# Performance work log

Measured on AMD Instinct MI355X. Metric: run time of the kernel, lower is better.

## Reference

```python
import jax, jax.numpy as jnp
import numpy as np


def setup_inputs() -> dict:
    key = jax.random.key(0)
    k_in, k_idx, k_neg, k_w, k_b = jax.random.split(key, 5)
    N, C_in, C_out, K, L = 8, 128, 256, 7, 16384
    x = jax.random.normal(k_in, (N, C_in, L), dtype=jnp.float32)
    idx = jax.random.randint(k_idx, (K, L), 0, L, dtype=jnp.int64)
    drop = jax.random.uniform(k_neg, (K, L)) < 0.05
    idx = jnp.where(drop, -1, idx)
    stdv = 1.0 / np.sqrt(C_in * K)
    weight = jax.random.uniform(k_w, (C_out, C_in, K), dtype=jnp.float32, minval=-stdv, maxval=stdv)
    bias = jax.random.uniform(k_b, (C_out,), dtype=jnp.float32, minval=-stdv, maxval=stdv)
    return {"input": x, "indices": idx, "weight": weight, "bias": bias}


def reference(input, indices, weight, bias):
    # indices: (K, L); -1 means zero-padding (matches utils.prepare_mask)
    mask = (indices >= 0).astype(input.dtype)          # (K, L)
    safe_idx = jnp.where(indices >= 0, indices, 0)     # (K, L)
    # im2col gather: (N, C_in, K, L), masked where neighbor is absent
    col = input[..., safe_idx] * mask
    # weight (C_out, C_in, K) contracted against col -> (N, C_out, L), mirrors bmm
    out = jnp.einsum('nckl,ock->nol', col, weight)
    out = out + bias[None, :, None]
    return out
```

## Files before the change

### kernel.cpp

```cpp
#include <hip/hip_runtime.h>
#include <stdint.h>

#define NB 8
#define CI 128
#define CO 256
#define KS 7
#define LL 16384
#define CK (CI * KS)

typedef _Float16 half8 __attribute__((ext_vector_type(8)));
typedef _Float16 half2v __attribute__((ext_vector_type(2)));
typedef float floatx4 __attribute__((ext_vector_type(4)));
typedef uint32_t uintx4 __attribute__((ext_vector_type(4)));

__device__ __forceinline__ void load16_to_lds(const void* g, void* l) {
    __builtin_amdgcn_global_load_lds(
        (const __attribute__((address_space(1))) void*)g,
        (__attribute__((address_space(3))) void*)l, 16, 0, 0);
}

__global__ __launch_bounds__(256) void convert_x(const float* __restrict__ x,
                                                 _Float16* __restrict__ xT) {
    __shared__ uint32_t tile[64][65];
    const int n  = blockIdx.y;
    const int l0 = blockIdx.x * 64;
    const int t  = threadIdx.x;
    const float* xs = x + (size_t)n * CI * LL + l0;

    const int l4  = (t & 15) * 4;
    const int cpr = t >> 4;
    #pragma unroll
    for (int p = 0; p < 4; ++p) {
        const int cp = cpr + p * 16;
        const float4 a4 = *(const float4*)(xs + (size_t)(2 * cp) * LL + l4);
        const float4 b4 = *(const float4*)(xs + (size_t)(2 * cp + 1) * LL + l4);
        half2v h;
        h[0] = (_Float16)a4.x; h[1] = (_Float16)b4.x;
        tile[l4 + 0][cp] = __builtin_bit_cast(uint32_t, h);
        h[0] = (_Float16)a4.y; h[1] = (_Float16)b4.y;
        tile[l4 + 1][cp] = __builtin_bit_cast(uint32_t, h);
        h[0] = (_Float16)a4.z; h[1] = (_Float16)b4.z;
        tile[l4 + 2][cp] = __builtin_bit_cast(uint32_t, h);
        h[0] = (_Float16)a4.w; h[1] = (_Float16)b4.w;
        tile[l4 + 3][cp] = __builtin_bit_cast(uint32_t, h);
    }
    __syncthreads();

    const int lw  = t >> 4;
    const int cp0 = (t & 15) * 4;
    _Float16* xd = xT + (size_t)n * LL * CI + (size_t)l0 * CI;
    #pragma unroll
    for (int p = 0; p < 4; ++p) {
        const int l = lw + p * 16;
        uintx4 d;
        d[0] = tile[l][cp0 + 0];
        d[1] = tile[l][cp0 + 1];
        d[2] = tile[l][cp0 + 2];
        d[3] = tile[l][cp0 + 3];
        *(uintx4*)(xd + (size_t)l * CI + cp0 * 2) = d;
    }
}

__global__ __launch_bounds__(256) void convert_w(const float* __restrict__ w,
                                                 _Float16* __restrict__ wT) {
    const int t = blockIdx.x * 256 + threadIdx.x;
    if (t >= CO * CK + 128) return;
    if (t >= CO * CK) { wT[t] = (_Float16)0.f; return; }
    const int o = t / CK;
    const int r = t - o * CK;
    const int k = r >> 7;
    const int c = r & 127;
    wT[t] = (_Float16)w[(size_t)o * CK + c * KS + k];
}

__global__ __launch_bounds__(256) void iconv_mfma(
    const _Float16* __restrict__ xT,
    const int*      __restrict__ idx,
    const _Float16* __restrict__ wT,
    const float*    __restrict__ bias,
    const _Float16* __restrict__ zrow,
    float*          __restrict__ out)
{
    __shared__ _Float16 a_lds[128 * 64];
    __shared__ _Float16 b_lds[128 * 64];

    const int l0 = blockIdx.x * 128;
    const int o0 = blockIdx.y * 128;
    const int n  = blockIdx.z;
    const int t  = threadIdx.x;
    const int lane = t & 63;
    const int wv = t >> 6;
    const int wo = (wv >> 1) * 64;
    const int wl = (wv & 1) * 64;
    const int m16 = lane & 15;
    const int q8  = (lane >> 4) * 8;

    floatx4 acc[4][4];
    #pragma unroll
    for (int i = 0; i < 4; ++i)
        #pragma unroll
        for (int j = 0; j < 4; ++j) acc[i][j] = (floatx4)0.f;

    const int srow = t >> 3;
    const int part = t & 7;

    int iv[KS][4];
    #pragma unroll
    for (int k = 0; k < KS; ++k)
        #pragma unroll
        for (int i = 0; i < 4; ++i)
            iv[k][i] = idx[k * LL + l0 + i * 32 + srow];

    const _Float16* xbase = xT + (size_t)n * LL * CI;
    const _Float16* wbase = wT + (size_t)(o0 + srow) * CK + part * 8;
    const int dst = srow * 64 + part * 8;

    for (int k = 0; k < KS; ++k) {
        for (int c0 = 0; c0 < CI; c0 += 64) {
            __syncthreads();
            #pragma unroll
            for (int i = 0; i < 4; ++i) {
                const int ii = iv[k][i];
                const _Float16* bs = (ii >= 0)
                    ? (xbase + (size_t)ii * CI + c0 + part * 8)
                    : (zrow + c0 + part * 8);
                load16_to_lds(bs, b_lds + i * 2048 + dst);
                load16_to_lds(wbase + (size_t)i * 32 * CK + k * CI + c0,
                              a_lds + i * 2048 + dst);
            }
            __syncthreads();

            #pragma unroll
            for (int kk = 0; kk < 2; ++kk) {
                half8 af[4], bf[4];
                #pragma unroll
                for (int mf = 0; mf < 4; ++mf)
                    af[mf] = *(const half8*)(a_lds + (wo + mf * 16 + m16) * 64 + kk * 32 + q8);
                #pragma unroll
                for (int nf = 0; nf < 4; ++nf)
                    bf[nf] = *(const half8*)(b_lds + (wl + nf * 16 + m16) * 64 + kk * 32 + q8);
                #pragma unroll
                for (int mf = 0; mf < 4; ++mf)
                    #pragma unroll
                    for (int nf = 0; nf < 4; ++nf)
                        acc[mf][nf] = __builtin_amdgcn_mfma_f32_16x16x32_f16(
                            af[mf], bf[nf], acc[mf][nf], 0, 0, 0);
            }
        }
    }

    const int r4 = (lane >> 4) * 4;
    #pragma unroll
    for (int mf = 0; mf < 4; ++mf) {
        const int obase = o0 + wo + mf * 16 + r4;
        const floatx4 b4 = *(const floatx4*)(bias + obase);
        #pragma unroll
        for (int nf = 0; nf < 4; ++nf) {
            const int l = l0 + wl + nf * 16 + m16;
            float* op = out + ((size_t)n * CO + obase) * LL + l;
            #pragma unroll
            for (int r = 0; r < 4; ++r)
                op[(size_t)r * LL] = acc[mf][nf][r] + b4[r];
        }
    }
}

__global__ __launch_bounds__(256) void iconv_fallback(
    const float* __restrict__ x, const int* __restrict__ idx,
    const float* __restrict__ w, const float* __restrict__ bias,
    float* __restrict__ out)
{
    __shared__ float col[CI][64];
    const int n  = blockIdx.y;
    const int l0 = blockIdx.x * 64;
    const int t  = threadIdx.x;
    const int ot = t & 63, lt = t >> 6;
    const int j = t >> 2, part = t & 3;
    float acc[4][16];
    #pragma unroll
    for (int oo = 0; oo < 4; ++oo) {
        const float bv = bias[ot * 4 + oo];
        #pragma unroll
        for (int ll = 0; ll < 16; ++ll) acc[oo][ll] = bv;
    }
    for (int k = 0; k < KS; ++k) {
        __syncthreads();
        const int i = idx[k * LL + l0 + j];
        const float* xr = x + (size_t)n * CI * LL;
        for (int q = 0; q < 32; ++q) {
            const int c = part * 32 + q;
            col[c][j] = (i >= 0) ? xr[(size_t)c * LL + i] : 0.f;
        }
        __syncthreads();
        for (int c = 0; c < CI; ++c) {
            const float* bv = &col[c][lt * 16];
            float wv[4];
            #pragma unroll
            for (int oo = 0; oo < 4; ++oo)
                wv[oo] = w[(size_t)(ot * 4 + oo) * CK + c * KS + k];
            #pragma unroll
            for (int oo = 0; oo < 4; ++oo)
                #pragma unroll
                for (int ll = 0; ll < 16; ++ll)
                    acc[oo][ll] += wv[oo] * bv[ll];
        }
    }
    #pragma unroll
    for (int oo = 0; oo < 4; ++oo) {
        float* orow = out + ((size_t)n * CO + (ot * 4 + oo)) * LL + l0 + lt * 16;
        #pragma unroll
        for (int q = 0; q < 16; ++q) orow[q] = acc[oo][q];
    }
}

extern "C" void kernel_launch(void* const* d_in, const int* in_sizes, int n_in,
                              void* d_out, int out_size, void* d_ws, size_t ws_size,
                              hipStream_t stream) {
    const float* x    = (const float*)d_in[0];
    const int*   idx  = (const int*)d_in[1];
    const float* w    = (const float*)d_in[2];
    const float* bias = (const float*)d_in[3];
    float* out = (float*)d_out;

    const size_t xt_bytes = (size_t)NB * LL * CI * sizeof(_Float16);
    const size_t wt_elems = (size_t)CO * CK + 128;
    const size_t need = xt_bytes + wt_elems * sizeof(_Float16);

    if (ws_size >= need) {
        _Float16* xT = (_Float16*)d_ws;
        _Float16* wT = (_Float16*)((char*)d_ws + xt_bytes);
        const _Float16* zr = wT + (size_t)CO * CK;
        convert_x<<<dim3(LL / 64, NB), 256, 0, stream>>>(x, xT);
        convert_w<<<dim3(((int)wt_elems + 255) / 256), 256, 0, stream>>>(w, wT);
        iconv_mfma<<<dim3(LL / 128, CO / 128, NB), 256, 0, stream>>>(
            xT, idx, wT, bias, zr, out);
    } else {
        iconv_fallback<<<dim3(LL / 64, NB), 256, 0, stream>>>(x, idx, w, bias, out);
    }
}
```

Measured before the change: 261.2 us.

## Double-buffer LDS tiles with swizzled layout and MFMA priority boost

Splits the A and B LDS tiles into two buffers so the global-to-LDS loads for the next K-chunk are issued before the MFMAs on the current chunk, with one barrier per iteration. Source chunks are XOR-swizzled by row so the half8 fragment reads hit fewer LDS bank conflicts, and s_setprio is raised around the MFMA block. The aim is to hide the gather latency and cut LDS conflicts. The cost is twice the LDS use (64KB per block), which may lower occupancy, and a fully unrolled 14-step loop that increases code size.

```diff
diff --git a/kernel.cpp b/kernel.cpp
--- a/kernel.cpp
+++ b/kernel.cpp
@@ -81,8 +81,8 @@
     const _Float16* __restrict__ zrow,
     float*          __restrict__ out)
 {
-    __shared__ _Float16 a_lds[128 * 64];
-    __shared__ _Float16 b_lds[128 * 64];
+    __shared__ _Float16 a_lds[2][128 * 64];
+    __shared__ _Float16 b_lds[2][128 * 64];
 
     const int l0 = blockIdx.x * 128;
     const int o0 = blockIdx.y * 128;
@@ -93,7 +93,8 @@
     const int wo = (wv >> 1) * 64;
     const int wl = (wv & 1) * 64;
     const int m16 = lane & 15;
-    const int q8  = (lane >> 4) * 8;
+    const int l4g = lane >> 4;
+    const int swz = (m16 & 7);
 
     floatx4 acc[4][4];
     #pragma unroll
@@ -103,6 +104,8 @@
 
     const int srow = t >> 3;
     const int part = t & 7;
+    const int sp   = (part ^ (srow & 7)) * 8;
+    const int dst  = srow * 64 + part * 8;
 
     int iv[KS][4];
     #pragma unroll
@@ -112,41 +115,64 @@
             iv[k][i] = idx[k * LL + l0 + i * 32 + srow];
 
     const _Float16* xbase = xT + (size_t)n * LL * CI;
-    const _Float16* wbase = wT + (size_t)(o0 + srow) * CK + part * 8;
-    const int dst = srow * 64 + part * 8;
-
-    for (int k = 0; k < KS; ++k) {
-        for (int c0 = 0; c0 < CI; c0 += 64) {
-            __syncthreads();
+    const _Float16* wbase = wT + (size_t)(o0 + srow) * CK;
+
+    {
+        const int k = 0, c0 = 0;
+        #pragma unroll
+        for (int i = 0; i < 4; ++i) {
+            const int ii = iv[k][i];
+            const _Float16* bs = (ii >= 0)
+                ? (xbase + (size_t)ii * CI + c0 + sp)
+                : (zrow + c0 + sp);
+            load16_to_lds(bs, &b_lds[0][i * 2048 + dst]);
+            load16_to_lds(wbase + (size_t)i * 32 * CK + k * CI + c0 + sp,
+                          &a_lds[0][i * 2048 + dst]);
+        }
+    }
+    __syncthreads();
+
+    #pragma unroll
+    for (int it = 0; it < 2 * KS; ++it) {
+        const int cur = it & 1;
+        if (it < 2 * KS - 1) {
+            const int nit = it + 1;
+            const int nk  = nit >> 1;
+            const int nc0 = (nit & 1) * 64;
+            const int nb  = nit & 1;
             #pragma unroll
             for (int i = 0; i < 4; ++i) {
-                const int ii = iv[k][i];
+                const int ii = iv[nk][i];
                 const _Float16* bs = (ii >= 0)
-                    ? (xbase + (size_t)ii * CI + c0 + part * 8)
-                    : (zrow + c0 + part * 8);
-                load16_to_lds(bs, b_lds + i * 2048 + dst);
-                load16_to_lds(wbase + (size_t)i * 32 * CK + k * CI + c0,
-                              a_lds + i * 2048 + dst);
+                    ? (xbase + (size_t)ii * CI + nc0 + sp)
+                    : (zrow + nc0 + sp);
+                load16_to_lds(bs, &b_lds[nb][i * 2048 + dst]);
+                load16_to_lds(wbase + (size_t)i * 32 * CK + nk * CI + nc0 + sp,
+                              &a_lds[nb][i * 2048 + dst]);
             }
-            __syncthreads();
-
-            #pragma unroll
-            for (int kk = 0; kk < 2; ++kk) {
-                half8 af[4], bf[4];
-                #pragma unroll
-                for (int mf = 0; mf < 4; ++mf)
-                    af[mf] = *(const half8*)(a_lds + (wo + mf * 16 + m16) * 64 + kk * 32 + q8);
+        }
+
+        #pragma unroll
+        for (int kk = 0; kk < 2; ++kk) {
+            const int ch = ((kk * 4 + l4g) ^ swz) * 8;
+            half8 af[4], bf[4];
+            #pragma unroll
+            for (int mf = 0; mf < 4; ++mf)
+                af[mf] = *(const half8*)(&a_lds[cur][(wo + mf * 16 + m16) * 64 + ch]);
+            #pragma unroll
+            for (int nf = 0; nf < 4; ++nf)
+                bf[nf] = *(const half8*)(&b_lds[cur][(wl + nf * 16 + m16) * 64 + ch]);
+            __builtin_amdgcn_s_setprio(1);
+            #pragma unroll
+            for (int mf = 0; mf < 4; ++mf)
                 #pragma unroll
                 for (int nf = 0; nf < 4; ++nf)
-                    bf[nf] = *(const half8*)(b_lds + (wl + nf * 16 + m16) * 64 + kk * 32 + q8);
-                #pragma unroll
-                for (int mf = 0; mf < 4; ++mf)
-                    #pragma unroll
-                    for (int nf = 0; nf < 4; ++nf)
-                        acc[mf][nf] = __builtin_amdgcn_mfma_f32_16x16x32_f16(
-                            af[mf], bf[nf], acc[mf][nf], 0, 0, 0);
-            }
-        }
+                    acc[mf][nf] = __builtin_amdgcn_mfma_f32_16x16x32_f16(
+                        af[mf], bf[nf], acc[mf][nf], 0, 0, 0);
+            __builtin_amdgcn_s_setprio(0);
+        }
+
+        __syncthreads();
     }
 
     const int r4 = (lane >> 4) * 4;
```

Result: faster. 247.3 us (-5.3%).

## Enlarge MFMA tile to 256x256, double-buffer LDS with swizzle and interleaved staging

Applied to the files above, without the earlier changes.

The gather-GEMM kernel now uses 512-thread blocks that each cover all 256 output channels and 256 positions, so each gathered input column is loaded once instead of twice. LDS is double-buffered, and the next stage's global-to-LDS loads are interleaved with four MFMA phases separated by barriers and priority hints, so loads overlap compute. An XOR swizzle on the LDS chunk offsets is meant to avoid bank conflicts. The trade-offs are 128 KB of LDS per block, 128 accumulator registers per thread, and fewer blocks in the grid, which limits occupancy.

```diff
diff --git a/kernel.cpp b/kernel.cpp
--- a/kernel.cpp
+++ b/kernel.cpp
@@ -73,7 +73,7 @@
     wT[t] = (_Float16)w[(size_t)o * CK + c * KS + k];
 }
 
-__global__ __launch_bounds__(256) void iconv_mfma(
+__global__ __launch_bounds__(512, 2) void iconv_mfma(
     const _Float16* __restrict__ xT,
     const int*      __restrict__ idx,
     const _Float16* __restrict__ wT,
@@ -81,78 +81,137 @@
     const _Float16* __restrict__ zrow,
     float*          __restrict__ out)
 {
-    __shared__ _Float16 a_lds[128 * 64];
-    __shared__ _Float16 b_lds[128 * 64];
-
-    const int l0 = blockIdx.x * 128;
-    const int o0 = blockIdx.y * 128;
+    __shared__ _Float16 a_lds[2][256 * 64];
+    __shared__ _Float16 b_lds[2][256 * 64];
+
+    const int l0 = blockIdx.x * 256;
     const int n  = blockIdx.z;
     const int t  = threadIdx.x;
     const int lane = t & 63;
-    const int wv = t >> 6;
-    const int wo = (wv >> 1) * 64;
-    const int wl = (wv & 1) * 64;
+    const int wv  = t >> 6;
+    const int wo  = (wv >> 2) * 128;
+    const int wl  = (wv & 3) * 64;
     const int m16 = lane & 15;
-    const int q8  = (lane >> 4) * 8;
-
-    floatx4 acc[4][4];
-    #pragma unroll
-    for (int i = 0; i < 4; ++i)
+    const int l4g = lane >> 4;
+    const int swz = m16 & 7;
+    const int ch0 = (l4g ^ swz) * 8;
+    const int ch1 = ((4 + l4g) ^ swz) * 8;
+
+    floatx4 acc[8][4];
+    #pragma unroll
+    for (int i = 0; i < 8; ++i)
         #pragma unroll
         for (int j = 0; j < 4; ++j) acc[i][j] = (floatx4)0.f;
 
-    const int srow = t >> 3;
+    const int rrow = t >> 3;
     const int part = t & 7;
+    const int sp   = (part ^ (rrow & 7)) * 8;
+    const int dstb = rrow * 64 + part * 8;
 
     int iv[KS][4];
     #pragma unroll
     for (int k = 0; k < KS; ++k)
         #pragma unroll
-        for (int i = 0; i < 4; ++i)
-            iv[k][i] = idx[k * LL + l0 + i * 32 + srow];
+        for (int j = 0; j < 4; ++j)
+            iv[k][j] = idx[k * LL + l0 + j * 64 + rrow];
 
     const _Float16* xbase = xT + (size_t)n * LL * CI;
-    const _Float16* wbase = wT + (size_t)(o0 + srow) * CK + part * 8;
-    const int dst = srow * 64 + part * 8;
-
-    for (int k = 0; k < KS; ++k) {
-        for (int c0 = 0; c0 < CI; c0 += 64) {
-            __syncthreads();
-            #pragma unroll
-            for (int i = 0; i < 4; ++i) {
-                const int ii = iv[k][i];
-                const _Float16* bs = (ii >= 0)
-                    ? (xbase + (size_t)ii * CI + c0 + part * 8)
-                    : (zrow + c0 + part * 8);
-                load16_to_lds(bs, b_lds + i * 2048 + dst);
-                load16_to_lds(wbase + (size_t)i * 32 * CK + k * CI + c0,
-                              a_lds + i * 2048 + dst);
-            }
-            __syncthreads();
-
-            #pragma unroll
-            for (int kk = 0; kk < 2; ++kk) {
-                half8 af[4], bf[4];
-                #pragma unroll
-                for (int mf = 0; mf < 4; ++mf)
-                    af[mf] = *(const half8*)(a_lds + (wo + mf * 16 + m16) * 64 + kk * 32 + q8);
-                #pragma unroll
-                for (int nf = 0; nf < 4; ++nf)
-                    bf[nf] = *(const half8*)(b_lds + (wl + nf * 16 + m16) * 64 + kk * 32 + q8);
-                #pragma unroll
-                for (int mf = 0; mf < 4; ++mf)
-                    #pragma unroll
-                    for (int nf = 0; nf < 4; ++nf)
-                        acc[mf][nf] = __builtin_amdgcn_mfma_f32_16x16x32_f16(
-                            af[mf], bf[nf], acc[mf][nf], 0, 0, 0);
-            }
-        }
-    }
+    const _Float16* abase = wT + (size_t)rrow * CK + sp;
+
+    #pragma unroll
+    for (int j = 0; j < 4; ++j) {
+        const int ii = iv[0][j];
+        const _Float16* bs = (ii >= 0) ? (xbase + (size_t)ii * CI + sp)
+                                       : (zrow + sp);
+        load16_to_lds(bs, &b_lds[0][j * 4096 + dstb]);
+        load16_to_lds(abase + (size_t)j * 64 * CK, &a_lds[0][j * 4096 + dstb]);
+    }
+    asm volatile("s_waitcnt vmcnt(0)" ::: "memory");
+    __builtin_amdgcn_s_barrier();
+
+#define RD_A(mh, ch)                                                              \
+    af[0] = *(const half8*)(&a_lds[cur][(wo + (mh)*64 +  0 + m16) * 64 + (ch)]);  \
+    af[1] = *(const half8*)(&a_lds[cur][(wo + (mh)*64 + 16 + m16) * 64 + (ch)]);  \
+    af[2] = *(const half8*)(&a_lds[cur][(wo + (mh)*64 + 32 + m16) * 64 + (ch)]);  \
+    af[3] = *(const half8*)(&a_lds[cur][(wo + (mh)*64 + 48 + m16) * 64 + (ch)]);
+
+#define RD_B(ch)                                                                  \
+    bf[0] = *(const half8*)(&b_lds[cur][(wl +  0 + m16) * 64 + (ch)]);            \
+    bf[1] = *(const half8*)(&b_lds[cur][(wl + 16 + m16) * 64 + (ch)]);            \
+    bf[2] = *(const half8*)(&b_lds[cur][(wl + 32 + m16) * 64 + (ch)]);            \
+    bf[3] = *(const half8*)(&b_lds[cur][(wl + 48 + m16) * 64 + (ch)]);
+
+#define STG_B(jj) do {                                                            \
+    const int ii = iv[k1][jj];                                                    \
+    const _Float16* bs = (ii >= 0) ? (xbase + (size_t)ii * CI + c1 + sp)          \
+                                   : (zrow + c1 + sp);                            \
+    load16_to_lds(bs, &b_lds[nb][(jj) * 4096 + dstb]); } while (0)
+
+#define STG_A(jj)                                                                 \
+    load16_to_lds(abase + (size_t)(jj) * 64 * CK + k1 * CI + c1,                  \
+                  &a_lds[nb][(jj) * 4096 + dstb])
+
+#define MFMA16(mh)                                                                \
+    __builtin_amdgcn_s_setprio(1);                                                \
+    _Pragma("unroll")                                                             \
+    for (int mf = 0; mf < 4; ++mf)                                                \
+        _Pragma("unroll")                                                         \
+        for (int nf = 0; nf < 4; ++nf)                                            \
+            acc[(mh)*4 + mf][nf] = __builtin_amdgcn_mfma_f32_16x16x32_f16(        \
+                af[mf], bf[nf], acc[(mh)*4 + mf][nf], 0, 0, 0);                   \
+    __builtin_amdgcn_s_setprio(0);
+
+#define PH_SYNC                                                                   \
+    __builtin_amdgcn_s_barrier();                                                 \
+    asm volatile("s_waitcnt lgkmcnt(0)" ::: "memory");                            \
+    __builtin_amdgcn_sched_barrier(0);
+
+    #pragma unroll
+    for (int s = 0; s < 2 * KS; ++s) {
+        const int cur = s & 1;
+        const int k1  = (s + 1) >> 1;
+        const int c1  = ((s + 1) & 1) * 64;
+        const int nb  = (s + 1) & 1;
+        half8 af[4], bf[4];
+
+        RD_A(0, ch0) RD_B(ch0)
+        if (s < 2 * KS - 1) { STG_B(0); STG_B(1); }
+        PH_SYNC
+        MFMA16(0)
+        __builtin_amdgcn_s_barrier();
+
+        RD_A(1, ch0)
+        if (s < 2 * KS - 1) { STG_B(2); STG_B(3); }
+        PH_SYNC
+        MFMA16(1)
+        __builtin_amdgcn_s_barrier();
+
+        RD_A(0, ch1) RD_B(ch1)
+        if (s < 2 * KS - 1) { STG_A(0); STG_A(1); }
+        PH_SYNC
+        MFMA16(0)
+        __builtin_amdgcn_s_barrier();
+
+        RD_A(1, ch1)
+        if (s < 2 * KS - 1) { STG_A(2); STG_A(3); }
+        PH_SYNC
+        MFMA16(1)
+        if (s < 2 * KS - 1)
+            asm volatile("s_waitcnt vmcnt(0)" ::: "memory");
+        __builtin_amdgcn_s_barrier();
+    }
+
+#undef RD_A
+#undef RD_B
+#undef STG_A
+#undef STG_B
+#undef MFMA16
+#undef PH_SYNC
 
     const int r4 = (lane >> 4) * 4;
     #pragma unroll
-    for (int mf = 0; mf < 4; ++mf) {
-        const int obase = o0 + wo + mf * 16 + r4;
+    for (int mf = 0; mf < 8; ++mf) {
+        const int obase = wo + mf * 16 + r4;
         const floatx4 b4 = *(const floatx4*)(bias + obase);
         #pragma unroll
         for (int nf = 0; nf < 4; ++nf) {
@@ -232,7 +291,7 @@
         const _Float16* zr = wT + (size_t)CO * CK;
         convert_x<<<dim3(LL / 64, NB), 256, 0, stream>>>(x, xT);
         convert_w<<<dim3(((int)wt_elems + 255) / 256), 256, 0, stream>>>(w, wT);
-        iconv_mfma<<<dim3(LL / 128, CO / 128, NB), 256, 0, stream>>>(
+        iconv_mfma<<<dim3(LL / 256, 1, NB), 512, 0, stream>>>(
             xT, idx, wT, bias, zr, out);
     } else {
         iconv_fallback<<<dim3(LL / 64, NB), 256, 0, stream>>>(x, idx, w, bias, out);
```

Measured after the change: 260.4 us. Within noise of the previous version (-0.3%).
